# Performance work log

Measured on AMD Instinct MI355X. Metric: run time of the kernel, lower is better.

## Reference

```python
import jax, jax.numpy as jnp
import numpy as np

EPS = 1e-5
H = 128
NA = 300000
NB = 600000
NBRS = 6

def _bn(x, gamma, beta):
    # BatchNorm1d in training mode: batch stats over dim 0, biased variance
    mu = jnp.mean(x, axis=0)
    var = jnp.mean((x - mu) ** 2, axis=0)
    return gamma * (x - mu) * jax.lax.rsqrt(var + EPS) + beta

def _lin(x, w, b):
    return x @ w.T + b

def setup_inputs() -> dict:
    key = jax.random.key(0)
    ks = jax.random.split(key, 20)
    s = 1.0 / np.sqrt(H)
    d = {
        'atom_layer_input': jax.random.normal(ks[0], (NA, H), jnp.float32),
        'bond_layer_input': jax.random.normal(ks[1], (NB, H), jnp.float32),
        'atom_adjacency_graph': jax.random.randint(ks[2], (NA, NBRS), 0, NA, jnp.int32),
        'atom_bond_adjacency_graph': jax.random.randint(ks[3], (NA, NBRS), 0, NB, jnp.int32),
        'bond_atom_adjacency_graph': jax.random.randint(ks[4], (NB, 2), 0, NA, jnp.int32),
    }
    names = ['U', 'V', 'A', 'B', 'C']
    for i, n in enumerate(names):
        d[n + '_w'] = jax.random.uniform(ks[5 + 2 * i], (H, H), jnp.float32, -s, s)
        d[n + '_b'] = jax.random.uniform(ks[6 + 2 * i], (H,), jnp.float32, -s, s)
    d['bn_bond_gamma'] = jnp.ones((H,), jnp.float32)
    d['bn_bond_beta'] = jnp.zeros((H,), jnp.float32)
    d['bn_atom_gamma'] = jnp.ones((H,), jnp.float32)
    d['bn_atom_beta'] = jnp.zeros((H,), jnp.float32)
    return d

def reference(atom_layer_input, bond_layer_input, atom_adjacency_graph,
              atom_bond_adjacency_graph, bond_atom_adjacency_graph,
              U_w, U_b, V_w, V_b, A_w, A_b, B_w, B_b, C_w, C_b,
              bn_bond_gamma, bn_bond_beta, bn_atom_gamma, bn_atom_beta):
    # --- edge (bond) update ---
    ex = atom_layer_input[bond_atom_adjacency_graph[:, 0]]  # [NB, H]
    ey = atom_layer_input[bond_atom_adjacency_graph[:, 1]]  # [NB, H]
    edge_syn = _lin(bond_layer_input, A_w, A_b) + _lin(ex, B_w, B_b) + _lin(ey, C_w, C_b)
    edge_gates = jax.nn.sigmoid(edge_syn)                    # [NB, H]
    edge_syn_bn = _bn(edge_syn, bn_bond_gamma, bn_bond_beta)
    bond_layer_output = jax.nn.relu(edge_syn_bn)             # residual overwritten in source
    # --- node (atom) update ---
    nbr_feats = atom_layer_input[atom_adjacency_graph]       # [NA, 6, H] gather
    nbr_V = jnp.einsum('nkh,oh->nko', nbr_feats, V_w) + V_b  # [NA, 6, H]
    nbr_gates = edge_gates[atom_bond_adjacency_graph]        # [NA, 6, H] gather
    msg = jnp.sum(nbr_gates * nbr_V, axis=1)                 # [NA, H]
    atom_syn = _lin(atom_layer_input, U_w, U_b) + msg
    atom_syn_bn = _bn(atom_syn, bn_atom_gamma, bn_atom_beta)
    atom_layer_output = jax.nn.relu(atom_syn_bn) + atom_layer_input  # residual (atom_feature_dim==0)
    return (atom_layer_output, bond_layer_output)
```

## Files before the change

### kernel.cpp

```cpp
#include <hip/hip_runtime.h>
#include <hip/hip_bf16.h>


#define H   128
#define NA  300000
#define NB  600000
#define EPS 1e-5f

#define NTILE_A (NA / 32)
#define NTILE_B (NB / 32)
#define GRID_A  1024
#define GRID_B  1024
#define EGRID   2048
#define LDSW    136

typedef __attribute__((ext_vector_type(4)))  float  f32x4;
typedef __attribute__((ext_vector_type(16))) float  f32x16;
typedef __attribute__((ext_vector_type(8)))  __bf16 bfv8;
typedef __attribute__((ext_vector_type(4)))  unsigned short u16x4;
typedef __attribute__((ext_vector_type(8)))  unsigned short u16x8;

static __device__ __forceinline__ unsigned short f2bf(float f) {
    unsigned u = __float_as_uint(f);
    u = (u + 0x7fffu + ((u >> 16) & 1u)) >> 16;
    return (unsigned short)u;
}
static __device__ __forceinline__ float bf2f(unsigned short s) {
    return __uint_as_float(((unsigned)s) << 16);
}

static __device__ __forceinline__ void bar_lds() {
    asm volatile("s_waitcnt lgkmcnt(0)\n\ts_barrier" ::: "memory");
}

static __device__ __forceinline__ u16x8 pack2(f32x4 a, f32x4 b) {
    u16x8 w;
#pragma unroll
    for (int i = 0; i < 4; i++) { w[i] = f2bf(a[i]); w[i + 4] = f2bf(b[i]); }
    return w;
}

static __device__ __forceinline__ bfv8 load_frag(const float* __restrict__ p) {
    f32x4 a = *(const f32x4*)p, b = *(const f32x4*)(p + 4);
    bfv8 f;
#pragma unroll
    for (int i = 0; i < 4; i++) { f[i] = (__bf16)a[i]; f[i + 4] = (__bf16)b[i]; }
    return f;
}

__global__ __launch_bounds__(512, 4) void k_atom_gemm(
    const float* __restrict__ X,
    const float* __restrict__ Uw, const float* __restrict__ Vw,
    unsigned short* __restrict__ Uxo, unsigned short* __restrict__ Vxo,
    unsigned short* __restrict__ Xbf)
{
    __shared__ unsigned short xs[2][32 * LDSW];
    __shared__ unsigned short es[2][32 * LDSW];

    const int tid   = threadIdx.x;
    const int lane  = tid & 63;
    const int w     = tid >> 6;
    const int ng    = w & 3;
    const int pair  = w >> 2;
    const int l31   = lane & 31;
    const int khalf = lane >> 5;

    const int wrow_off = (ng * 32 + l31) * H + khalf * 8;
    const int cperm    = ng * 32 + khalf * 16;

    const float* W = pair ? Vw : Uw;
    bfv8 aw[8];
#pragma unroll
    for (int k = 0; k < 8; k++) aw[k] = load_frag(W + wrow_off + k * 16);

    const int srow = tid >> 4, sseg = tid & 15;
    const int g = tid >> 8, ft = tid & 255;
    const int frow = ft >> 3, fseg = ft & 7;
    unsigned short* O = g ? Vxo : Uxo;

    const int stride = gridDim.x;
    int t = blockIdx.x;

    f32x4 sl0, sl1;
    {
        const float* sp = X + (size_t)(t * 32 + srow) * H + sseg * 8;
        sl0 = *(const f32x4*)sp; sl1 = *(const f32x4*)(sp + 4);
        u16x8 pk = pack2(sl0, sl1);
        *(u16x8*)&xs[0][srow * LDSW + sseg * 8] = pk;
        *(u16x8*)(Xbf + (size_t)(t * 32 + srow) * H + sseg * 8) = pk;
    }
    __syncthreads();

    int p = 0;
#pragma unroll 1
    for (; t < NTILE_A; ) {
        const int tn = t + stride;
        const bool have = tn < NTILE_A;
        if (have) {
            const float* sp = X + (size_t)(tn * 32 + srow) * H + sseg * 8;
            sl0 = *(const f32x4*)sp; sl1 = *(const f32x4*)(sp + 4);
        }

        {
            const unsigned short* xrow = &xs[p][l31 * LDSW + khalf * 8];
            f32x16 acc;
#pragma unroll
            for (int i = 0; i < 16; i++) acc[i] = 0.0f;
#pragma unroll
            for (int k = 0; k < 8; k++) {
                bfv8 xf = *(const bfv8*)(xrow + k * 16);
                acc = __builtin_amdgcn_mfma_f32_32x32x16_bf16(aw[k], xf, acc, 0, 0, 0);
            }
            u16x8 o0, o1;
#pragma unroll
            for (int v = 0; v < 8; v++) { o0[v] = f2bf(acc[v]); o1[v] = f2bf(acc[v + 8]); }
            unsigned short* esw = &es[pair][l31 * LDSW + cperm];
            *(u16x8*)esw       = o0;
            *(u16x8*)(esw + 8) = o1;
        }
        bar_lds();

        {
            const unsigned short* esr = &es[g][frow * LDSW + fseg * 16];
            u16x8 e0 = *(const u16x8*)esr, e1 = *(const u16x8*)(esr + 8);
            const size_t fbase = (size_t)(t * 32 + frow) * H + fseg * 16;
            *(u16x8*)(O + fbase)     = e0;
            *(u16x8*)(O + fbase + 8) = e1;
        }
        if (have) {
            u16x8 pk = pack2(sl0, sl1);
            *(u16x8*)&xs[p ^ 1][srow * LDSW + sseg * 8] = pk;
            *(u16x8*)(Xbf + (size_t)(tn * 32 + srow) * H + sseg * 8) = pk;
        }
        bar_lds();
        p ^= 1;
        t = tn;
    }
}

__global__ __launch_bounds__(256, 2) void k_bond_gemm(
    const float* __restrict__ Xb, const unsigned short* __restrict__ Xbf,
    const float* __restrict__ Aw, const float* __restrict__ Bw,
    const float* __restrict__ Cw,
    const float* __restrict__ Ab, const float* __restrict__ Bb,
    const float* __restrict__ Cb,
    const int* __restrict__ g2,
    unsigned short* __restrict__ esyn,
    float* __restrict__ psum, float* __restrict__ psq)
{
    __shared__ unsigned short ts[3][32 * LDSW];
    __shared__ unsigned short es[32 * LDSW];
    __shared__ float bias_s[128];

    const int tid   = threadIdx.x;
    const int lane  = tid & 63;
    const int ng    = tid >> 6;
    const int l31   = lane & 31;
    const int khalf = lane >> 5;
    const int cperm = ng * 32 + khalf * 16;

    const int wro = (ng * 32 + l31) * H + khalf * 8;
    bfv8 awA[8], awB[8], awC[8];
#pragma unroll
    for (int k = 0; k < 8; k++) {
        awA[k] = load_frag(Aw + wro + k * 16);
        awB[k] = load_frag(Bw + wro + k * 16);
        awC[k] = load_frag(Cw + wro + k * 16);
    }

    if (tid < 128) {
        const int pcol = tid;
        const int grp = pcol >> 5, r = pcol & 31, kh = r >> 4, wi = r & 15;
        const int ct = grp * 32 + (wi >> 2) * 8 + kh * 4 + (wi & 3);
        bias_s[pcol] = Ab[ct] + Bb[ct] + Cb[ct];
    }

    const int srow = tid >> 3, sseg = tid & 7;

    float fs[16], fq[16];
#pragma unroll
    for (int i = 0; i < 16; i++) { fs[i] = 0.f; fq[i] = 0.f; }

    const int stride = gridDim.x;
    int t = blockIdx.x;

    f32x4 sxb[4];
    u16x8 re0, re1, ry0, ry1;
    int2 gg;

    {
        int2 g0 = *(const int2*)(g2 + 2 * (size_t)(t * 32 + srow));
        const float* sp = Xb + (size_t)(t * 32 + srow) * H + sseg * 16;
#pragma unroll
        for (int i = 0; i < 4; i++) sxb[i] = *(const f32x4*)(sp + 4 * i);
        const unsigned short* ep = Xbf + (size_t)g0.x * H + sseg * 16;
        re0 = *(const u16x8*)ep;  re1 = *(const u16x8*)(ep + 8);
        const unsigned short* yp = Xbf + (size_t)g0.y * H + sseg * 16;
        ry0 = *(const u16x8*)yp;  ry1 = *(const u16x8*)(yp + 8);
        const int tnx = t + stride;
        if (tnx < NTILE_B) gg = *(const int2*)(g2 + 2 * (size_t)(tnx * 32 + srow));
    }

#pragma unroll 1
    for (; t < NTILE_B; ) {
        const int tn = t + stride;
        const bool have = tn < NTILE_B;

        {
            const int off = srow * LDSW + sseg * 16;
            *(u16x8*)&ts[0][off]     = pack2(sxb[0], sxb[1]);
            *(u16x8*)&ts[0][off + 8] = pack2(sxb[2], sxb[3]);
            *(u16x8*)&ts[1][off]     = re0; *(u16x8*)&ts[1][off + 8] = re1;
            *(u16x8*)&ts[2][off]     = ry0; *(u16x8*)&ts[2][off + 8] = ry1;
        }
        bar_lds();

        if (have) {
            const float* sp = Xb + (size_t)(tn * 32 + srow) * H + sseg * 16;
#pragma unroll
            for (int i = 0; i < 4; i++) sxb[i] = *(const f32x4*)(sp + 4 * i);
            const unsigned short* ep = Xbf + (size_t)gg.x * H + sseg * 16;
            re0 = *(const u16x8*)ep;  re1 = *(const u16x8*)(ep + 8);
            const unsigned short* yp = Xbf + (size_t)gg.y * H + sseg * 16;
            ry0 = *(const u16x8*)yp;  ry1 = *(const u16x8*)(yp + 8);
            const int tnn = tn + stride;
            if (tnn < NTILE_B) gg = *(const int2*)(g2 + 2 * (size_t)(tnn * 32 + srow));
        }

        {
            const unsigned short* x0 = &ts[0][l31 * LDSW + khalf * 8];
            const unsigned short* x1 = &ts[1][l31 * LDSW + khalf * 8];
            const unsigned short* x2 = &ts[2][l31 * LDSW + khalf * 8];
            f32x16 acc;
#pragma unroll
            for (int i = 0; i < 16; i++) acc[i] = 0.0f;
#pragma unroll
            for (int k = 0; k < 8; k++)
                acc = __builtin_amdgcn_mfma_f32_32x32x16_bf16(awA[k], *(const bfv8*)(x0 + k * 16), acc, 0, 0, 0);
#pragma unroll
            for (int k = 0; k < 8; k++)
                acc = __builtin_amdgcn_mfma_f32_32x32x16_bf16(awB[k], *(const bfv8*)(x1 + k * 16), acc, 0, 0, 0);
#pragma unroll
            for (int k = 0; k < 8; k++)
                acc = __builtin_amdgcn_mfma_f32_32x32x16_bf16(awC[k], *(const bfv8*)(x2 + k * 16), acc, 0, 0, 0);
            u16x8 o0, o1;
#pragma unroll
            for (int v = 0; v < 8; v++) { o0[v] = f2bf(acc[v]); o1[v] = f2bf(acc[v + 8]); }
            unsigned short* esw = &es[l31 * LDSW + cperm];
            *(u16x8*)esw       = o0;
            *(u16x8*)(esw + 8) = o1;
        }
        bar_lds();

        {
            const unsigned short* esr = &es[srow * LDSW + sseg * 16];
            u16x8 e0 = *(const u16x8*)esr, e1 = *(const u16x8*)(esr + 8);
            const float* bp = bias_s + sseg * 16;
            u16x8 w0, w1;
#pragma unroll
            for (int i = 0; i < 8; i++) {
                float v = bf2f(e0[i]) + bp[i];
                w0[i] = f2bf(v); fs[i] += v; fq[i] += v * v;
            }
#pragma unroll
            for (int i = 0; i < 8; i++) {
                float v = bf2f(e1[i]) + bp[8 + i];
                w1[i] = f2bf(v); fs[8 + i] += v; fq[8 + i] += v * v;
            }
            unsigned short* op = esyn + (size_t)(t * 32 + srow) * H + sseg * 16;
            *(u16x8*)op       = w0;
            *(u16x8*)(op + 8) = w1;
        }
        t = tn;
    }

    float* red = (float*)es;
    for (int i = 0; i < 16; i++) {
        __syncthreads();
        red[tid] = fs[i]; red[256 + tid] = fq[i];
        __syncthreads();
        if (tid < 8) {
            float S = 0.f, Q = 0.f;
            for (int r = 0; r < 32; r++) { S += red[r * 8 + tid]; Q += red[256 + r * 8 + tid]; }
            psum[(size_t)blockIdx.x * H + tid * 16 + i] = S;
            psq [(size_t)blockIdx.x * H + tid * 16 + i] = Q;
        }
    }
}

__global__ void k_bn_stats(const float* __restrict__ psum, const float* __restrict__ psq,
                           int nblk, float invN,
                           const float* __restrict__ gamma, const float* __restrict__ beta,
                           float* __restrict__ scale, float* __restrict__ shift)
{
    __shared__ float ls[256], lq[256];
    const int c = blockIdx.x;
    float s = 0.f, q = 0.f;
    for (int i = threadIdx.x; i < nblk; i += 256) {
        s += psum[(size_t)i * H + c];
        q += psq [(size_t)i * H + c];
    }
    ls[threadIdx.x] = s; lq[threadIdx.x] = q;
    __syncthreads();
    for (int off = 128; off > 0; off >>= 1) {
        if ((int)threadIdx.x < off) {
            ls[threadIdx.x] += ls[threadIdx.x + off];
            lq[threadIdx.x] += lq[threadIdx.x + off];
        }
        __syncthreads();
    }
    if (threadIdx.x == 0) {
        const int r = c & 31, kh = r >> 4, wi = r & 15;
        const int ct = (c & ~31) + (wi >> 2) * 8 + kh * 4 + (wi & 3);
        float mean = ls[0] * invN;
        float var  = lq[0] * invN - mean * mean;
        float sc   = gamma[ct] * rsqrtf(var + EPS);
        scale[c] = sc;
        shift[c] = beta[ct] - mean * sc;
    }
}

__global__ __launch_bounds__(256) void k_bond_out(const unsigned short* __restrict__ esyn,
                                                  float* __restrict__ y,
                                                  const float* __restrict__ scale,
                                                  const float* __restrict__ shift)
{
    const size_t total  = (size_t)NB * (H / 8);
    const size_t stride = (size_t)gridDim.x * 256;
    const int c0 = (threadIdx.x & 15) * 8;
    const f32x4 sc0 = *(const f32x4*)(scale + c0), sc1 = *(const f32x4*)(scale + c0 + 4);
    const f32x4 sh0 = *(const f32x4*)(shift + c0), sh1 = *(const f32x4*)(shift + c0 + 4);
    const int tc0 = (c0 & ~31) + (((c0 >> 2) & 3) * 8) + ((c0 >> 4) & 1) * 4;
    const int tc1 = tc0 + 8;
    for (size_t i = (size_t)blockIdx.x * 256 + threadIdx.x; i < total; i += stride) {
        u16x8 v = ((const u16x8*)esyn)[i];
        const size_t row = i >> 4;
        f32x4 o0, o1;
#pragma unroll
        for (int j = 0; j < 4; j++) {
            o0[j] = fmaxf(bf2f(v[j])     * sc0[j] + sh0[j], 0.0f);
            o1[j] = fmaxf(bf2f(v[j + 4]) * sc1[j] + sh1[j], 0.0f);
        }
        float* yp = y + row * H;
        *(f32x4*)(yp + tc0) = o0;
        *(f32x4*)(yp + tc1) = o1;
    }
}

__global__ __launch_bounds__(256) void k_atom_msg(
    const unsigned short* __restrict__ Ux,
    const unsigned short* __restrict__ Vx,
    const unsigned short* __restrict__ esyn,
    const int* __restrict__ adj,
    const int* __restrict__ abadj,
    const float* __restrict__ Ub, const float* __restrict__ Vb,
    unsigned short* __restrict__ syn_a,
    float* __restrict__ psum, float* __restrict__ psq)
{
    const int cg = threadIdx.x & 15;
    const int rh = threadIdx.x >> 4;
    const int c0 = cg * 8;
    const int tc0 = (c0 & ~31) + (((c0 >> 2) & 3) * 8) + ((c0 >> 4) & 1) * 4;
    const f32x4 ub0 = *(const f32x4*)(Ub + tc0), ub1 = *(const f32x4*)(Ub + tc0 + 8);
    const f32x4 vb0 = *(const f32x4*)(Vb + tc0), vb1 = *(const f32x4*)(Vb + tc0 + 8);

    float s[8], q[8];
#pragma unroll
    for (int j = 0; j < 8; j++) { s[j] = 0.f; q[j] = 0.f; }

    const int rstride = gridDim.x * 16;
    int r = blockIdx.x * 16 + rh;

    int2 A[3], Bv[3];
    if (r < NA) {
#pragma unroll
        for (int p = 0; p < 3; p++) {
            A[p]  = *(const int2*)(adj   + (size_t)r * 6 + 2 * p);
            Bv[p] = *(const int2*)(abadj + (size_t)r * 6 + 2 * p);
        }
    }

#pragma unroll 1
    for (; r < NA; ) {
        const int rn = r + rstride;

        const int ai[6] = {A[0].x, A[0].y, A[1].x, A[1].y, A[2].x, A[2].y};
        const int bi[6] = {Bv[0].x, Bv[0].y, Bv[1].x, Bv[1].y, Bv[2].x, Bv[2].y};

        u16x8 uv = *(const u16x8*)(Ux + (size_t)r * H + c0);

        if (rn < NA) {
#pragma unroll
            for (int p = 0; p < 3; p++) {
                A[p]  = *(const int2*)(adj   + (size_t)rn * 6 + 2 * p);
                Bv[p] = *(const int2*)(abadj + (size_t)rn * 6 + 2 * p);
            }
        }

        float v[8];
#pragma unroll
        for (int j = 0; j < 4; j++) {
            v[j]     = bf2f(uv[j])     + ub0[j];
            v[j + 4] = bf2f(uv[j + 4]) + ub1[j];
        }
#pragma unroll
        for (int k = 0; k < 6; k++) {
            u16x8 vx = *(const u16x8*)(Vx   + (size_t)ai[k] * H + c0);
            u16x8 es = *(const u16x8*)(esyn + (size_t)bi[k] * H + c0);
#pragma unroll
            for (int j = 0; j < 4; j++) {
                float g0 = 1.0f / (1.0f + __expf(-bf2f(es[j])));
                float g1 = 1.0f / (1.0f + __expf(-bf2f(es[j + 4])));
                v[j]     += g0 * (bf2f(vx[j])     + vb0[j]);
                v[j + 4] += g1 * (bf2f(vx[j + 4]) + vb1[j]);
            }
        }
        u16x8 ov;
#pragma unroll
        for (int j = 0; j < 8; j++) ov[j] = f2bf(v[j]);
        *(u16x8*)(syn_a + (size_t)r * H + c0) = ov;
#pragma unroll
        for (int j = 0; j < 8; j++) { s[j] += v[j]; q[j] += v[j] * v[j]; }

        r = rn;
    }

    __shared__ float ls[256][8], lq[256][8];
#pragma unroll
    for (int j = 0; j < 8; j++) { ls[threadIdx.x][j] = s[j]; lq[threadIdx.x][j] = q[j]; }
    __syncthreads();
    if (threadIdx.x < 128) {
        const int c = threadIdx.x, g = c >> 3, j = c & 7;
        float S = 0.f, Q = 0.f;
        for (int rg = 0; rg < 16; rg++) { S += ls[rg * 16 + g][j]; Q += lq[rg * 16 + g][j]; }
        psum[(size_t)blockIdx.x * H + c] = S;
        psq [(size_t)blockIdx.x * H + c] = Q;
    }
}

__global__ __launch_bounds__(256) void k_atom_out(const unsigned short* __restrict__ syn,
                                                  const unsigned short* __restrict__ xbf,
                                                  float* __restrict__ y,
                                                  const float* __restrict__ scale,
                                                  const float* __restrict__ shift)
{
    const size_t total  = (size_t)NA * (H / 8);
    const size_t stride = (size_t)gridDim.x * 256;
    const int c0 = (threadIdx.x & 15) * 8;
    const f32x4 sc0 = *(const f32x4*)(scale + c0), sc1 = *(const f32x4*)(scale + c0 + 4);
    const f32x4 sh0 = *(const f32x4*)(shift + c0), sh1 = *(const f32x4*)(shift + c0 + 4);
    const int tc0 = (c0 & ~31) + (((c0 >> 2) & 3) * 8) + ((c0 >> 4) & 1) * 4;
    const int tc1 = tc0 + 8;
    for (size_t i = (size_t)blockIdx.x * 256 + threadIdx.x; i < total; i += stride) {
        u16x8 v = ((const u16x8*)syn)[i];
        const size_t row = i >> 4;
        const unsigned short* xp = xbf + row * H;
        u16x4 x0 = *(const u16x4*)(xp + tc0);
        u16x4 x1 = *(const u16x4*)(xp + tc1);
        f32x4 o0, o1;
#pragma unroll
        for (int j = 0; j < 4; j++) {
            o0[j] = fmaxf(bf2f(v[j])     * sc0[j] + sh0[j], 0.0f) + bf2f(x0[j]);
            o1[j] = fmaxf(bf2f(v[j + 4]) * sc1[j] + sh1[j], 0.0f) + bf2f(x1[j]);
        }
        float* yp = y + row * H;
        *(f32x4*)(yp + tc0) = o0;
        *(f32x4*)(yp + tc1) = o1;
    }
}

extern "C" void kernel_launch(void* const* d_in, const int* in_sizes, int n_in,
                              void* d_out, int out_size, void* d_ws, size_t ws_size,
                              hipStream_t stream)
{
    const float* X     = (const float*)d_in[0];
    const float* Xb    = (const float*)d_in[1];
    const int*   adj   = (const int*)d_in[2];
    const int*   abadj = (const int*)d_in[3];
    const int*   g2    = (const int*)d_in[4];
    const float* Uw = (const float*)d_in[5],  *Ub = (const float*)d_in[6];
    const float* Vw = (const float*)d_in[7],  *Vb = (const float*)d_in[8];
    const float* Aw = (const float*)d_in[9],  *Ab = (const float*)d_in[10];
    const float* Bw = (const float*)d_in[11], *Bb = (const float*)d_in[12];
    const float* Cw = (const float*)d_in[13], *Cb = (const float*)d_in[14];
    const float* gb = (const float*)d_in[15], *bb = (const float*)d_in[16];
    const float* ga = (const float*)d_in[17], *ba = (const float*)d_in[18];

    float* out_atom = (float*)d_out;
    float* out_bond = out_atom + (size_t)NA * H;

    char* ws = (char*)d_ws;
    size_t o = 0;
    unsigned short* Ux    = (unsigned short*)(ws + o); o += (size_t)NA * H * 2;
    unsigned short* Vx    = (unsigned short*)(ws + o); o += (size_t)NA * H * 2;
    unsigned short* Xbf   = (unsigned short*)(ws + o); o += (size_t)NA * H * 2;
    unsigned short* esyn  = (unsigned short*)(ws + o); o += (size_t)NB * H * 2;
    unsigned short* syn_a = (unsigned short*)(ws + o); o += (size_t)NA * H * 2;
    float* psum_b = (float*)(ws + o);  o += (size_t)EGRID * H * 4;
    float* psq_b  = (float*)(ws + o);  o += (size_t)EGRID * H * 4;
    float* psum_a = (float*)(ws + o);  o += (size_t)EGRID * H * 4;
    float* psq_a  = (float*)(ws + o);  o += (size_t)EGRID * H * 4;
    float* scale_b = (float*)(ws + o); o += 512;
    float* shift_b = (float*)(ws + o); o += 512;
    float* scale_a = (float*)(ws + o); o += 512;
    float* shift_a = (float*)(ws + o); o += 512;
    (void)o; (void)ws_size; (void)in_sizes; (void)n_in; (void)out_size;

    k_atom_gemm<<<GRID_A, 512, 0, stream>>>(X, Uw, Vw, Ux, Vx, Xbf);
    k_bond_gemm<<<GRID_B, 256, 0, stream>>>(Xb, Xbf, Aw, Bw, Cw, Ab, Bb, Cb, g2,
                                            esyn, psum_b, psq_b);
    k_bn_stats<<<H, 256, 0, stream>>>(psum_b, psq_b, GRID_B, 1.0f / NB, gb, bb, scale_b, shift_b);
    k_bond_out<<<EGRID, 256, 0, stream>>>(esyn, out_bond, scale_b, shift_b);
    k_atom_msg<<<EGRID, 256, 0, stream>>>(Ux, Vx, esyn, adj, abadj, Ub, Vb, syn_a, psum_a, psq_a);
    k_bn_stats<<<H, 256, 0, stream>>>(psum_a, psq_a, EGRID, 1.0f / NA, ga, ba, scale_a, shift_a);
    k_atom_out<<<EGRID, 256, 0, stream>>>(syn_a, Xbf, out_atom, scale_a, shift_a);
}
```

Baseline: 560.2 us.

## Merge bond output and atom message kernels into one block-partitioned launch

Combines the bond BN/ReLU output kernel and the atom message-passing kernel into a single launch. The first 512 blocks write the bond output and the remaining 1536 blocks do the gather-heavy atom messages. Both stages depend only on esyn, so they can run concurrently instead of one after the other, which removes one launch and the tail gap between them. The fixed block split may leave one side idle while the other is still running, and the message part now has fewer blocks than before.

```diff
diff --git a/kernel.cpp b/kernel.cpp
--- a/kernel.cpp
+++ b/kernel.cpp
@@ -12,6 +12,9 @@
 #define GRID_A  1024
 #define GRID_B  1024
 #define EGRID   2048
+#define BOUT_BLKS 512
+#define MSG_BLKS  1536
+#define FUSED_GRID (BOUT_BLKS + MSG_BLKS)
 #define LDSW    136
 
 typedef __attribute__((ext_vector_type(4)))  float  f32x4;
@@ -320,43 +323,45 @@
     }
 }
 
-__global__ __launch_bounds__(256) void k_bond_out(const unsigned short* __restrict__ esyn,
-                                                  float* __restrict__ y,
-                                                  const float* __restrict__ scale,
-                                                  const float* __restrict__ shift)
-{
-    const size_t total  = (size_t)NB * (H / 8);
-    const size_t stride = (size_t)gridDim.x * 256;
-    const int c0 = (threadIdx.x & 15) * 8;
-    const f32x4 sc0 = *(const f32x4*)(scale + c0), sc1 = *(const f32x4*)(scale + c0 + 4);
-    const f32x4 sh0 = *(const f32x4*)(shift + c0), sh1 = *(const f32x4*)(shift + c0 + 4);
-    const int tc0 = (c0 & ~31) + (((c0 >> 2) & 3) * 8) + ((c0 >> 4) & 1) * 4;
-    const int tc1 = tc0 + 8;
-    for (size_t i = (size_t)blockIdx.x * 256 + threadIdx.x; i < total; i += stride) {
-        u16x8 v = ((const u16x8*)esyn)[i];
-        const size_t row = i >> 4;
-        f32x4 o0, o1;
-#pragma unroll
-        for (int j = 0; j < 4; j++) {
-            o0[j] = fmaxf(bf2f(v[j])     * sc0[j] + sh0[j], 0.0f);
-            o1[j] = fmaxf(bf2f(v[j + 4]) * sc1[j] + sh1[j], 0.0f);
-        }
-        float* yp = y + row * H;
-        *(f32x4*)(yp + tc0) = o0;
-        *(f32x4*)(yp + tc1) = o1;
-    }
-}
-
-__global__ __launch_bounds__(256) void k_atom_msg(
+__global__ __launch_bounds__(256) void k_bout_amsg(
+    const unsigned short* __restrict__ esyn,
+    float* __restrict__ out_bond,
+    const float* __restrict__ scale, const float* __restrict__ shift,
     const unsigned short* __restrict__ Ux,
     const unsigned short* __restrict__ Vx,
-    const unsigned short* __restrict__ esyn,
     const int* __restrict__ adj,
     const int* __restrict__ abadj,
     const float* __restrict__ Ub, const float* __restrict__ Vb,
     unsigned short* __restrict__ syn_a,
     float* __restrict__ psum, float* __restrict__ psq)
 {
+    __shared__ float ls[256][8], lq[256][8];
+
+    if (blockIdx.x < BOUT_BLKS) {
+        const size_t total  = (size_t)NB * (H / 8);
+        const size_t stride = (size_t)BOUT_BLKS * 256;
+        const int c0 = (threadIdx.x & 15) * 8;
+        const f32x4 sc0 = *(const f32x4*)(scale + c0), sc1 = *(const f32x4*)(scale + c0 + 4);
+        const f32x4 sh0 = *(const f32x4*)(shift + c0), sh1 = *(const f32x4*)(shift + c0 + 4);
+        const int tc0 = (c0 & ~31) + (((c0 >> 2) & 3) * 8) + ((c0 >> 4) & 1) * 4;
+        const int tc1 = tc0 + 8;
+        for (size_t i = (size_t)blockIdx.x * 256 + threadIdx.x; i < total; i += stride) {
+            u16x8 v = ((const u16x8*)esyn)[i];
+            const size_t row = i >> 4;
+            f32x4 o0, o1;
+#pragma unroll
+            for (int j = 0; j < 4; j++) {
+                o0[j] = fmaxf(bf2f(v[j])     * sc0[j] + sh0[j], 0.0f);
+                o1[j] = fmaxf(bf2f(v[j + 4]) * sc1[j] + sh1[j], 0.0f);
+            }
+            float* yp = out_bond + row * H;
+            *(f32x4*)(yp + tc0) = o0;
+            *(f32x4*)(yp + tc1) = o1;
+        }
+        return;
+    }
+
+    const int bid = blockIdx.x - BOUT_BLKS;
     const int cg = threadIdx.x & 15;
     const int rh = threadIdx.x >> 4;
     const int c0 = cg * 8;
@@ -368,8 +373,8 @@
 #pragma unroll
     for (int j = 0; j < 8; j++) { s[j] = 0.f; q[j] = 0.f; }
 
-    const int rstride = gridDim.x * 16;
-    int r = blockIdx.x * 16 + rh;
+    const int rstride = MSG_BLKS * 16;
+    int r = bid * 16 + rh;
 
     int2 A[3], Bv[3];
     if (r < NA) {
@@ -425,7 +430,6 @@
         r = rn;
     }
 
-    __shared__ float ls[256][8], lq[256][8];
 #pragma unroll
     for (int j = 0; j < 8; j++) { ls[threadIdx.x][j] = s[j]; lq[threadIdx.x][j] = q[j]; }
     __syncthreads();
@@ -433,8 +437,8 @@
         const int c = threadIdx.x, g = c >> 3, j = c & 7;
         float S = 0.f, Q = 0.f;
         for (int rg = 0; rg < 16; rg++) { S += ls[rg * 16 + g][j]; Q += lq[rg * 16 + g][j]; }
-        psum[(size_t)blockIdx.x * H + c] = S;
-        psq [(size_t)blockIdx.x * H + c] = Q;
+        psum[(size_t)bid * H + c] = S;
+        psq [(size_t)bid * H + c] = Q;
     }
 }
 
@@ -510,8 +514,9 @@
     k_bond_gemm<<<GRID_B, 256, 0, stream>>>(Xb, Xbf, Aw, Bw, Cw, Ab, Bb, Cb, g2,
                                             esyn, psum_b, psq_b);
     k_bn_stats<<<H, 256, 0, stream>>>(psum_b, psq_b, GRID_B, 1.0f / NB, gb, bb, scale_b, shift_b);
-    k_bond_out<<<EGRID, 256, 0, stream>>>(esyn, out_bond, scale_b, shift_b);
-    k_atom_msg<<<EGRID, 256, 0, stream>>>(Ux, Vx, esyn, adj, abadj, Ub, Vb, syn_a, psum_a, psq_a);
-    k_bn_stats<<<H, 256, 0, stream>>>(psum_a, psq_a, EGRID, 1.0f / NA, ga, ba, scale_a, shift_a);
+    k_bout_amsg<<<FUSED_GRID, 256, 0, stream>>>(esyn, out_bond, scale_b, shift_b,
+                                                Ux, Vx, adj, abadj, Ub, Vb,
+                                                syn_a, psum_a, psq_a);
+    k_bn_stats<<<H, 256, 0, stream>>>(psum_a, psq_a, MSG_BLKS, 1.0f / NA, ga, ba, scale_a, shift_a);
     k_atom_out<<<EGRID, 256, 0, stream>>>(syn_a, Xbf, out_atom, scale_a, shift_a);
 }
```

Measured after the change: 536.9 us (median of 2 runs). -4.2%, faster.
